# Kernel optimization log

Measured on AMD Instinct MI355X. Metric: run time of the kernel, lower is better.

Reference implementation:

```python
import jax, jax.numpy as jnp
import numpy as np


def setup_inputs() -> dict:
    key = jax.random.key(0)
    k1, k2 = jax.random.split(key)
    data = jax.random.normal(k1, (1000000, 64), dtype=jnp.float32)
    # unique, in-range indices (ONNX ScatterND is undefined for duplicates)
    indices = jnp.arange(100000, dtype=jnp.int64 if jax.config.jax_enable_x64 else jnp.int32).reshape(100000, 1)
    updates = jax.random.normal(k2, (100000, 64), dtype=jnp.float32)
    return {"data": data, "indices": indices, "updates": updates}


def reference(data, indices, updates):
    # ONNX ScatterND with k = indices.shape[-1] = 1: scatter rows of `updates`
    # into a copy of `data` at row positions indices[..., 0].
    rows = indices[..., 0]  # [num_updates]
    return data.at[rows].set(updates)
```

## Files before the change

### kernel.cpp

```cpp
#include <hip/hip_runtime.h>


__global__ void scatternd_copy_kernel(const float4* __restrict__ src,
                                      float4* __restrict__ dst,
                                      size_t n4) {
    size_t i = (size_t)blockIdx.x * blockDim.x + threadIdx.x;
    const size_t stride = (size_t)gridDim.x * blockDim.x;
    for (; i < n4; i += stride) {
        dst[i] = src[i];
    }
}

__global__ void scatternd_scatter_kernel(const int* __restrict__ idx,
                                         const float4* __restrict__ upd,
                                         float4* __restrict__ out,
                                         size_t total4) {
    size_t i = (size_t)blockIdx.x * blockDim.x + threadIdx.x;
    const size_t stride = (size_t)gridDim.x * blockDim.x;
    for (; i < total4; i += stride) {
        const size_t row = i >> 4;
        const size_t col = i & 15;
        const int r = idx[row];
        out[(size_t)r * 16 + col] = upd[i];
    }
}

extern "C" void kernel_launch(void* const* d_in, const int* in_sizes, int n_in,
                              void* d_out, int out_size, void* d_ws, size_t ws_size,
                              hipStream_t stream) {
    const float* data    = (const float*)d_in[0];
    const int*   indices = (const int*)d_in[1];
    const float* updates = (const float*)d_in[2];
    float* out = (float*)d_out;

    const size_t n4 = (size_t)out_size / 4;
    const size_t num_updates = (size_t)in_sizes[1];
    const size_t total4 = num_updates * 16;

    const int block = 256;
    int grid_copy = (int)((n4 + block - 1) / block);
    if (grid_copy > 2048) grid_copy = 2048;
    int grid_scat = (int)((total4 + block - 1) / block);
    if (grid_scat > 2048) grid_scat = 2048;

    scatternd_copy_kernel<<<grid_copy, block, 0, stream>>>(
        (const float4*)data, (float4*)out, n4);
    scatternd_scatter_kernel<<<grid_scat, block, 0, stream>>>(
        indices, (const float4*)updates, (float4*)out, total4);
}
```

Before: 114.1 us.

## Skip copying overwritten rows using a scatter flag array

Reorders the work so the scatter runs first and marks written rows in a byte flag array in workspace. A following copy pass copies only rows not overwritten, avoiding redundant reads and writes of rows that are replaced by updates. The copy loop is also unrolled four-way for memory-level parallelism. It costs an extra zeroing launch and flag reads, and falls back to the old path if workspace is too small.

Result: no change. 114.9 us (+0.6%).

```diff
diff --git a/kernel.cpp b/kernel.cpp
--- a/kernel.cpp
+++ b/kernel.cpp
@@ -1,20 +1,66 @@
 #include <hip/hip_runtime.h>
+#include <stdint.h>
 
 
-__global__ void scatternd_copy_kernel(const float4* __restrict__ src,
-                                      float4* __restrict__ dst,
-                                      size_t n4) {
+__global__ void zero_bytes_kernel(uint4* __restrict__ p, size_t n16) {
     size_t i = (size_t)blockIdx.x * blockDim.x + threadIdx.x;
     const size_t stride = (size_t)gridDim.x * blockDim.x;
-    for (; i < n4; i += stride) {
-        dst[i] = src[i];
+    for (; i < n16; i += stride) p[i] = make_uint4(0u, 0u, 0u, 0u);
+}
+
+__global__ void scatter_flag_kernel(const int* __restrict__ idx,
+                                    const float4* __restrict__ upd,
+                                    float4* __restrict__ out,
+                                    uint8_t* __restrict__ flags,
+                                    size_t total4) {
+    size_t i = (size_t)blockIdx.x * blockDim.x + threadIdx.x;
+    const size_t stride = (size_t)gridDim.x * blockDim.x;
+    for (; i < total4; i += stride) {
+        const size_t row = i >> 4;
+        const size_t col = i & 15;
+        const int r = idx[row];
+        out[(size_t)r * 16 + col] = upd[i];
+        if (col == 0) flags[r] = 1;
     }
 }
 
-__global__ void scatternd_scatter_kernel(const int* __restrict__ idx,
-                                         const float4* __restrict__ upd,
-                                         float4* __restrict__ out,
-                                         size_t total4) {
+__global__ void copy_skip_kernel(const float4* __restrict__ src,
+                                 float4* __restrict__ dst,
+                                 const uint8_t* __restrict__ flags,
+                                 size_t n4) {
+    const size_t stride = (size_t)gridDim.x * blockDim.x;
+    size_t i = (size_t)blockIdx.x * blockDim.x + threadIdx.x;
+    for (; i + 3 * stride < n4; i += 4 * stride) {
+        const size_t i0 = i, i1 = i + stride, i2 = i + 2 * stride, i3 = i + 3 * stride;
+        const bool c0 = !flags[i0 >> 4];
+        const bool c1 = !flags[i1 >> 4];
+        const bool c2 = !flags[i2 >> 4];
+        const bool c3 = !flags[i3 >> 4];
+        float4 v0, v1, v2, v3;
+        if (c0) v0 = src[i0];
+        if (c1) v1 = src[i1];
+        if (c2) v2 = src[i2];
+        if (c3) v3 = src[i3];
+        if (c0) dst[i0] = v0;
+        if (c1) dst[i1] = v1;
+        if (c2) dst[i2] = v2;
+        if (c3) dst[i3] = v3;
+    }
+    for (; i < n4; i += stride) {
+        if (!flags[i >> 4]) dst[i] = src[i];
+    }
+}
+
+__global__ void copy_all_kernel(const float4* __restrict__ src,
+                                float4* __restrict__ dst, size_t n4) {
+    size_t i = (size_t)blockIdx.x * blockDim.x + threadIdx.x;
+    const size_t stride = (size_t)gridDim.x * blockDim.x;
+    for (; i < n4; i += stride) dst[i] = src[i];
+}
+
+__global__ void scatter_kernel(const int* __restrict__ idx,
+                               const float4* __restrict__ upd,
+                               float4* __restrict__ out, size_t total4) {
     size_t i = (size_t)blockIdx.x * blockDim.x + threadIdx.x;
     const size_t stride = (size_t)gridDim.x * blockDim.x;
     for (; i < total4; i += stride) {
@@ -33,18 +79,30 @@
     const float* updates = (const float*)d_in[2];
     float* out = (float*)d_out;
 
-    const size_t n4 = (size_t)out_size / 4;
-    const size_t num_updates = (size_t)in_sizes[1];
-    const size_t total4 = num_updates * 16;
+    const size_t n4          = (size_t)out_size / 4;
+    const size_t num_rows    = (size_t)out_size / 64;
+    const size_t num_updates = (size_t)in_sizes[2] / 64;
+    const size_t total4      = num_updates * 16;
 
     const int block = 256;
-    int grid_copy = (int)((n4 + block - 1) / block);
-    if (grid_copy > 2048) grid_copy = 2048;
-    int grid_scat = (int)((total4 + block - 1) / block);
-    if (grid_scat > 2048) grid_scat = 2048;
+    auto grid_for = [&](size_t work) {
+        size_t g = (work + block - 1) / block;
+        if (g > 2048) g = 2048;
+        return (int)g;
+    };
 
-    scatternd_copy_kernel<<<grid_copy, block, 0, stream>>>(
-        (const float4*)data, (float4*)out, n4);
-    scatternd_scatter_kernel<<<grid_scat, block, 0, stream>>>(
-        indices, (const float4*)updates, (float4*)out, total4);
+    if (ws_size >= num_rows && (num_rows % 16) == 0) {
+        uint8_t* flags = (uint8_t*)d_ws;
+        const size_t n16 = num_rows / 16;
+        zero_bytes_kernel<<<grid_for(n16), block, 0, stream>>>((uint4*)d_ws, n16);
+        scatter_flag_kernel<<<grid_for(total4), block, 0, stream>>>(
+            indices, (const float4*)updates, (float4*)out, flags, total4);
+        copy_skip_kernel<<<grid_for(n4 / 4), block, 0, stream>>>(
+            (const float4*)data, (float4*)out, flags, n4);
+    } else {
+        copy_all_kernel<<<grid_for(n4), block, 0, stream>>>(
+            (const float4*)data, (float4*)out, n4);
+        scatter_kernel<<<grid_for(total4), block, 0, stream>>>(
+            indices, (const float4*)updates, (float4*)out, total4);
+    }
 }
```

## Fuse copy and scatter via inverse-index permutation into single write pass

Applied to the files above, without the earlier changes.

Builds an inverse map from output row to update row in workspace (memset to -1, then a scatter kernel), and a fused kernel writes each output element once, sourcing from updates or data. This avoids writing scattered rows twice and reading the overwritten data rows, and uses nontemporal loads/stores with 4x unrolling. It adds a memset, an extra launch and per-element perm lookups, and falls back to the old path if the workspace is too small.

New measurement: 115.8 us. Within noise of the previous version (+1.4%).

```diff
diff --git a/kernel.cpp b/kernel.cpp
--- a/kernel.cpp
+++ b/kernel.cpp
@@ -1,20 +1,60 @@
 #include <hip/hip_runtime.h>
+#include <stdint.h>
 
 
-__global__ void scatternd_copy_kernel(const float4* __restrict__ src,
-                                      float4* __restrict__ dst,
-                                      size_t n4) {
+typedef float f32x4 __attribute__((ext_vector_type(4)));
+
+__global__ void scatter_perm_kernel(const int* __restrict__ idx,
+                                    int* __restrict__ perm, int n) {
+    int t = blockIdx.x * blockDim.x + threadIdx.x;
+    if (t < n) perm[idx[t]] = t;
+}
+
+__global__ __launch_bounds__(256) void fused_write_kernel(
+    const f32x4* __restrict__ data,
+    const f32x4* __restrict__ upd,
+    const int* __restrict__ perm,
+    f32x4* __restrict__ out,
+    size_t n4) {
+    const size_t stride = (size_t)gridDim.x * blockDim.x;
     size_t i = (size_t)blockIdx.x * blockDim.x + threadIdx.x;
-    const size_t stride = (size_t)gridDim.x * blockDim.x;
+
+    for (; i + 3 * stride < n4; i += 4 * stride) {
+        const size_t i0 = i, i1 = i + stride, i2 = i + 2 * stride, i3 = i + 3 * stride;
+        const int j0 = perm[i0 >> 4];
+        const int j1 = perm[i1 >> 4];
+        const int j2 = perm[i2 >> 4];
+        const int j3 = perm[i3 >> 4];
+        const f32x4* s0 = (j0 >= 0) ? (upd + ((size_t)j0 * 16 + (i0 & 15))) : (data + i0);
+        const f32x4* s1 = (j1 >= 0) ? (upd + ((size_t)j1 * 16 + (i1 & 15))) : (data + i1);
+        const f32x4* s2 = (j2 >= 0) ? (upd + ((size_t)j2 * 16 + (i2 & 15))) : (data + i2);
+        const f32x4* s3 = (j3 >= 0) ? (upd + ((size_t)j3 * 16 + (i3 & 15))) : (data + i3);
+        f32x4 v0 = __builtin_nontemporal_load(s0);
+        f32x4 v1 = __builtin_nontemporal_load(s1);
+        f32x4 v2 = __builtin_nontemporal_load(s2);
+        f32x4 v3 = __builtin_nontemporal_load(s3);
+        __builtin_nontemporal_store(v0, out + i0);
+        __builtin_nontemporal_store(v1, out + i1);
+        __builtin_nontemporal_store(v2, out + i2);
+        __builtin_nontemporal_store(v3, out + i3);
+    }
     for (; i < n4; i += stride) {
-        dst[i] = src[i];
+        const int j = perm[i >> 4];
+        const f32x4* s = (j >= 0) ? (upd + ((size_t)j * 16 + (i & 15))) : (data + i);
+        __builtin_nontemporal_store(__builtin_nontemporal_load(s), out + i);
     }
 }
 
-__global__ void scatternd_scatter_kernel(const int* __restrict__ idx,
-                                         const float4* __restrict__ upd,
-                                         float4* __restrict__ out,
-                                         size_t total4) {
+__global__ void copy_all_kernel(const f32x4* __restrict__ src,
+                                f32x4* __restrict__ dst, size_t n4) {
+    size_t i = (size_t)blockIdx.x * blockDim.x + threadIdx.x;
+    const size_t stride = (size_t)gridDim.x * blockDim.x;
+    for (; i < n4; i += stride) dst[i] = src[i];
+}
+
+__global__ void scatter_kernel(const int* __restrict__ idx,
+                               const f32x4* __restrict__ upd,
+                               f32x4* __restrict__ out, size_t total4) {
     size_t i = (size_t)blockIdx.x * blockDim.x + threadIdx.x;
     const size_t stride = (size_t)gridDim.x * blockDim.x;
     for (; i < total4; i += stride) {
@@ -33,18 +73,29 @@
     const float* updates = (const float*)d_in[2];
     float* out = (float*)d_out;
 
-    const size_t n4 = (size_t)out_size / 4;
-    const size_t num_updates = (size_t)in_sizes[1];
-    const size_t total4 = num_updates * 16;
+    const size_t n4          = (size_t)out_size / 4;
+    const size_t num_rows    = (size_t)out_size / 64;
+    const size_t num_updates = (size_t)in_sizes[2] / 64;
 
     const int block = 256;
-    int grid_copy = (int)((n4 + block - 1) / block);
-    if (grid_copy > 2048) grid_copy = 2048;
-    int grid_scat = (int)((total4 + block - 1) / block);
-    if (grid_scat > 2048) grid_scat = 2048;
+    auto grid_for = [&](size_t work) {
+        size_t g = (work + block - 1) / block;
+        if (g > 2048) g = 2048;
+        return (int)g;
+    };
 
-    scatternd_copy_kernel<<<grid_copy, block, 0, stream>>>(
-        (const float4*)data, (float4*)out, n4);
-    scatternd_scatter_kernel<<<grid_scat, block, 0, stream>>>(
-        indices, (const float4*)updates, (float4*)out, total4);
+    if (ws_size >= num_rows * sizeof(int)) {
+        int* perm = (int*)d_ws;
+        (void)hipMemsetAsync(perm, 0xFF, num_rows * sizeof(int), stream);
+        scatter_perm_kernel<<<grid_for(num_updates), block, 0, stream>>>(
+            indices, perm, (int)num_updates);
+        fused_write_kernel<<<grid_for(n4 / 4), block, 0, stream>>>(
+            (const f32x4*)data, (const f32x4*)updates, perm, (f32x4*)out, n4);
+    } else {
+        const size_t total4 = num_updates * 16;
+        copy_all_kernel<<<grid_for(n4), block, 0, stream>>>(
+            (const f32x4*)data, (f32x4*)out, n4);
+        scatter_kernel<<<grid_for(total4), block, 0, stream>>>(
+            indices, (const f32x4*)updates, (f32x4*)out, total4);
+    }
 }
```
